# Kernel tuning notes

Measured on AMD Instinct MI355X. Metric: run time of the kernel, lower is better.

The kernel has to match this reference:

```python
import jax, jax.numpy as jnp
import numpy as np


def _three_nn(parent_xyz, xyz):
    # parent_xyz: (bs, n, 3) queries; xyz: (bs, m, 3) reference points.
    # Squared pairwise distances (bs, n, m) without forming (x-y)^2 tensor of rank 4.
    d2 = (jnp.sum(parent_xyz**2, -1, keepdims=True)
          - 2.0 * jnp.einsum('bnd,bmd->bnm', parent_xyz, xyz)
          + jnp.sum(xyz**2, -1)[:, None, :])
    neg_d2, idx = jax.lax.top_k(-d2, 3)           # 3 smallest distances
    dist = jnp.sqrt(jnp.maximum(-neg_d2, 0.0))    # pointnet2 returns sqrt(dist2)
    return dist, idx                              # (bs, n, 3), (bs, n, 3)


def _three_interpolate(feats, idx, weight):
    # feats: (bs, c, m); idx, weight: (bs, n, 3) -> (bs, c, n)
    feats_t = jnp.swapaxes(feats, 1, 2)                     # (bs, m, c)
    gathered = jax.vmap(lambda f, i: f[i])(feats_t, idx)    # (bs, n, 3, c)
    out = jnp.einsum('bnkc,bnk->bcn', gathered, weight)
    return out


def _conv1x1(x, W, b):
    # x: (bs, c_in, n); W: (c_out, c_in); b: (c_out,)
    return jnp.einsum('oc,bcn->bon', W, x) + b[None, :, None]


def setup_inputs() -> dict:
    key = jax.random.key(0)
    ks = jax.random.split(key, 6)
    bs, m, n = 8, 1024, 4096
    c0, c1, c2 = 256, 128, 256
    xyz = jax.random.normal(ks[0], (bs, m, 3), jnp.float32)
    parent_xyz = jax.random.normal(ks[1], (bs, n, 3), jnp.float32)
    feats = jax.random.normal(ks[2], (bs, c0, m), jnp.float32)
    skip_feats = jax.random.normal(ks[3], (bs, c1, n), jnp.float32)
    W1 = jax.random.normal(ks[4], (c2, c0 + c1), jnp.float32) * (1.0 / np.sqrt(c0 + c1))
    b1 = jnp.zeros((c2,), jnp.float32)
    W2 = jax.random.normal(ks[5], (c2, c2), jnp.float32) * (1.0 / np.sqrt(c2))
    b2 = jnp.zeros((c2,), jnp.float32)
    return {"xyz": xyz, "parent_xyz": parent_xyz, "feats": feats,
            "skip_feats": skip_feats, "W1": W1, "b1": b1, "W2": W2, "b2": b2}


def reference(xyz, parent_xyz, feats, skip_feats, W1, b1, W2, b2):
    dist, idx = _three_nn(parent_xyz, xyz)
    inv_dist = 1.0 / (dist + 1e-8)
    weight = inv_dist / jnp.sum(inv_dist, 2, keepdims=True)     # (bs, n, 3)
    up_feats = _three_interpolate(feats, idx, weight)           # (bs, c0, n)
    parent_feats = jnp.concatenate([up_feats, skip_feats], 1)   # (bs, c0+c1, n)
    h = jax.nn.relu(_conv1x1(parent_feats, W1, b1))
    out = jax.nn.relu(_conv1x1(h, W2, b2))
    return out
```

## Files before the change

### kernel.cpp

```cpp
#include <hip/hip_runtime.h>
#include <hip/hip_bf16.h>
#include <cstddef>
#include <cstdint>

#define BS    8
#define M_PTS 1024
#define N_PTS 4096
#define C0    256
#define C1    128
#define C2    256
#define K1DIM 384

typedef __attribute__((ext_vector_type(8))) short bf16x8;
typedef __attribute__((ext_vector_type(4))) float f32x4;

__device__ __forceinline__ ushort f2bf(float f) {
  union { float f; unsigned u; } v; v.f = f;
  unsigned r = v.u + 0x7fffu + ((v.u >> 16) & 1u);
  return (ushort)(r >> 16);
}

__device__ __forceinline__ int pfbu(int kq, int n) {
  return kq * 64 + (n ^ (kq & 7));
}

__global__ void transpose_k(const float* __restrict__ in, float* __restrict__ out,
                            int R, int C) {
  __shared__ float tile[32][33];
  const int b  = blockIdx.z;
  const int r0 = blockIdx.y * 32, c0 = blockIdx.x * 32;
  const int tx = threadIdx.x, ty = threadIdx.y;
  const float* ip = in  + (size_t)b * R * C;
  float*       op = out + (size_t)b * R * C;
#pragma unroll
  for (int i = 0; i < 4; ++i) {
    int r = r0 + ty + i * 8, c = c0 + tx;
    if (r < R && c < C) tile[ty + i * 8][tx] = ip[(size_t)r * C + c];
  }
  __syncthreads();
#pragma unroll
  for (int i = 0; i < 4; ++i) {
    int c = c0 + ty + i * 8, r = r0 + tx;
    if (r < R && c < C) op[(size_t)c * R + r] = tile[tx][ty + i * 8];
  }
}

__global__ __launch_bounds__(256) void wprep_k(
    const float* __restrict__ W1, const float* __restrict__ W2,
    ushort* __restrict__ W1f, ushort* __restrict__ W2f) {
  const int id = blockIdx.x * 256 + threadIdx.x;
  if (id < C2 * K1DIM) {
    int m = id / K1DIM, k = id - m * K1DIM;
    int off = (((m >> 4) * 12 + (k >> 5)) * 4 + ((k >> 3) & 3)) * 128 + (m & 15) * 8 + (k & 7);
    W1f[off] = f2bf(W1[id]);
  }
  if (id < C2 * C2) {
    int m = id >> 8, k = id & 255;
    int off = (((m >> 4) * 8 + (k >> 5)) * 4 + ((k >> 3) & 3)) * 128 + (m & 15) * 8 + (k & 7);
    W2f[off] = f2bf(W2[id]);
  }
}

__global__ __launch_bounds__(512, 4) void fp_fused_k(
    const float* __restrict__ xyz,
    const float* __restrict__ pxyz,
    const float* __restrict__ featsT,
    const float* __restrict__ skip,
    const ushort* __restrict__ W1f,
    const float* __restrict__ b1,
    const ushort* __restrict__ W2f,
    const float* __restrict__ b2,
    float* __restrict__ out) {
  __shared__ float4 smem4[3072];
  __shared__ int   idx_s[64][3];
  __shared__ float w_s[64][3];

  float4* pts = smem4;
  float*  md  = (float*)smem4 + 4128;
  int*    mi  = (int*)smem4  + 4128 + 1536;
  ushort* pfB = (ushort*)smem4;

  const int t  = threadIdx.x;
  const int b  = blockIdx.x & 7;
  const int n0 = (blockIdx.x >> 3) * 64;

  for (int m = t; m < M_PTS; m += 512) {
    const float x = xyz[(size_t)b * 3 * M_PTS + 3 * m + 0];
    const float y = xyz[(size_t)b * 3 * M_PTS + 3 * m + 1];
    const float z = xyz[(size_t)b * 3 * M_PTS + 3 * m + 2];
    const float s2 = __fadd_rn(__fadd_rn(__fmul_rn(x, x), __fmul_rn(y, y)),
                               __fmul_rn(z, z));
    pts[m + (m >> 7)] = (float4){x, y, z, s2};
  }
  __syncthreads();

  float skp[16];
#pragma unroll
  for (int it = 0; it < 8; ++it) {
    const int id = t + it * 512;
    const int r2 = id >> 6, nn = id & 63;
    skp[2 * it + 0] = skip[((size_t)b * C1 + 2 * r2 + 0) * N_PTS + n0 + nn];
    skp[2 * it + 1] = skip[((size_t)b * C1 + 2 * r2 + 1) * N_PTS + n0 + nn];
  }

  {
    const int q = t >> 3, sub = t & 7;
    const int gn = n0 + q;
    const float qx = pxyz[((size_t)b * N_PTS + gn) * 3 + 0];
    const float qy = pxyz[((size_t)b * N_PTS + gn) * 3 + 1];
    const float qz = pxyz[((size_t)b * N_PTS + gn) * 3 + 2];
    const float qq = __fadd_rn(__fadd_rn(__fmul_rn(qx, qx), __fmul_rn(qy, qy)),
                               __fmul_rn(qz, qz));
    float d0 = 3.4e38f, d1 = 3.4e38f, d2 = 3.4e38f;
    int   i0 = 0, i1 = 0, i2 = 0;
    const int mbase = sub * 128;
    const int pbase = mbase + sub;
    for (int it = 0; it < 128; ++it) {
      const float4 P = pts[pbase + it];
      const float dot = __fadd_rn(__fadd_rn(__fmul_rn(qx, P.x), __fmul_rn(qy, P.y)),
                                  __fmul_rn(qz, P.z));
      const float d = __fadd_rn(__fsub_rn(qq, __fmul_rn(2.0f, dot)), P.w);
      const int m = mbase + it;
      if (d < d0)      { d2 = d1; i2 = i1; d1 = d0; i1 = i0; d0 = d; i0 = m; }
      else if (d < d1) { d2 = d1; i2 = i1; d1 = d;  i1 = m; }
      else if (d < d2) { d2 = d;  i2 = m; }
    }
    const int base = (q * 8 + sub) * 3;
    md[base + 0] = d0; md[base + 1] = d1; md[base + 2] = d2;
    mi[base + 0] = i0; mi[base + 1] = i1; mi[base + 2] = i2;

    if (sub == 0) {
      float e0 = 3.4e38f, e1 = 3.4e38f, e2 = 3.4e38f;
      int   j0 = 0, j1 = 0, j2 = 0;
#pragma unroll
      for (int s = 0; s < 8; ++s)
#pragma unroll
        for (int k = 0; k < 3; ++k) {
          float d = md[(q * 8 + s) * 3 + k]; int m = mi[(q * 8 + s) * 3 + k];
          if (d < e0)      { e2 = e1; j2 = j1; e1 = e0; j1 = j0; e0 = d; j0 = m; }
          else if (d < e1) { e2 = e1; j2 = j1; e1 = d;  j1 = m; }
          else if (d < e2) { e2 = d;  j2 = m; }
        }
      float t0 = sqrtf(fmaxf(e0, 0.f)), t1 = sqrtf(fmaxf(e1, 0.f)),
            t2 = sqrtf(fmaxf(e2, 0.f));
      float r0 = 1.0f / (t0 + 1e-8f), r1 = 1.0f / (t1 + 1e-8f),
            r2 = 1.0f / (t2 + 1e-8f);
      float rs = __fadd_rn(__fadd_rn(r0, r1), r2);
      idx_s[q][0] = j0; idx_s[q][1] = j1; idx_s[q][2] = j2;
      w_s[q][0] = r0 / rs; w_s[q][1] = r1 / rs; w_s[q][2] = r2 / rs;
    }
  }
  __syncthreads();

  const int wv = t >> 6, l = t & 63;

  {
    const float* fb = featsT + (size_t)b * M_PTS * C0;
#pragma unroll
    for (int qi = 0; qi < 8; ++qi) {
      const int nq = wv * 8 + qi;
      const float w0 = w_s[nq][0], w1 = w_s[nq][1], w2 = w_s[nq][2];
      const float4 f0 = *(const float4*)(fb + (size_t)idx_s[nq][0] * C0 + l * 4);
      const float4 f1 = *(const float4*)(fb + (size_t)idx_s[nq][1] * C0 + l * 4);
      const float4 f2 = *(const float4*)(fb + (size_t)idx_s[nq][2] * C0 + l * 4);
      ushort4 hv;
      hv.x = f2bf(w0 * f0.x + w1 * f1.x + w2 * f2.x);
      hv.y = f2bf(w0 * f0.y + w1 * f1.y + w2 * f2.y);
      hv.z = f2bf(w0 * f0.z + w1 * f1.z + w2 * f2.z);
      hv.w = f2bf(w0 * f0.w + w1 * f1.w + w2 * f2.w);
      *reinterpret_cast<ushort4*>(&pfB[pfbu(l >> 1, nq) * 8 + (l & 1) * 4]) = hv;
    }
  }
#pragma unroll
  for (int it = 0; it < 8; ++it) {
    const int id = t + it * 512;
    const int r2 = id >> 6, nn = id & 63;
    ushort2 sv; sv.x = f2bf(skp[2 * it]); sv.y = f2bf(skp[2 * it + 1]);
    const int k = C0 + 2 * r2;
    *reinterpret_cast<ushort2*>(&pfB[pfbu(k >> 3, nn) * 8 + (k & 7)]) = sv;
  }
  __syncthreads();

  const int c = l & 15, g = l >> 4;

  f32x4 acc[2][4];
#pragma unroll
  for (int i = 0; i < 2; ++i)
#pragma unroll
    for (int j = 0; j < 4; ++j) acc[i][j] = (f32x4){0.f, 0.f, 0.f, 0.f};

  for (int kb = 0; kb < 12; ++kb) {
    bf16x8 bfr[4], afr[2];
#pragma unroll
    for (int j = 0; j < 4; ++j)
      bfr[j] = *reinterpret_cast<const bf16x8*>(&pfB[pfbu(kb * 4 + g, j * 16 + c) * 8]);
#pragma unroll
    for (int i = 0; i < 2; ++i)
      afr[i] = *reinterpret_cast<const bf16x8*>(&W1f[(((2 * wv + i) * 12 + kb) * 4 + g) * 128 + c * 8]);
#pragma unroll
    for (int i = 0; i < 2; ++i)
#pragma unroll
      for (int j = 0; j < 4; ++j)
        acc[i][j] = __builtin_amdgcn_mfma_f32_16x16x32_bf16(afr[i], bfr[j], acc[i][j], 0, 0, 0);
  }
  __syncthreads();

#pragma unroll
  for (int i = 0; i < 2; ++i) {
    const int mbase = wv * 32 + i * 16 + g * 4;
    const float4 bias = *(const float4*)(b1 + mbase);
#pragma unroll
    for (int j = 0; j < 4; ++j) {
      const int nn = j * 16 + c;
      ushort4 hv;
      hv.x = f2bf(fmaxf(acc[i][j].x + bias.x, 0.f));
      hv.y = f2bf(fmaxf(acc[i][j].y + bias.y, 0.f));
      hv.z = f2bf(fmaxf(acc[i][j].z + bias.z, 0.f));
      hv.w = f2bf(fmaxf(acc[i][j].w + bias.w, 0.f));
      *reinterpret_cast<ushort4*>(&pfB[pfbu(mbase >> 3, nn) * 8 + (mbase & 7)]) = hv;
    }
  }
  __syncthreads();

#pragma unroll
  for (int i = 0; i < 2; ++i)
#pragma unroll
    for (int j = 0; j < 4; ++j) acc[i][j] = (f32x4){0.f, 0.f, 0.f, 0.f};

  for (int kb = 0; kb < 8; ++kb) {
    bf16x8 bfr[4], afr[2];
#pragma unroll
    for (int j = 0; j < 4; ++j)
      bfr[j] = *reinterpret_cast<const bf16x8*>(&pfB[pfbu(kb * 4 + g, j * 16 + c) * 8]);
#pragma unroll
    for (int i = 0; i < 2; ++i)
      afr[i] = *reinterpret_cast<const bf16x8*>(&W2f[(((2 * wv + i) * 8 + kb) * 4 + g) * 128 + c * 8]);
#pragma unroll
    for (int i = 0; i < 2; ++i)
#pragma unroll
      for (int j = 0; j < 4; ++j)
        acc[i][j] = __builtin_amdgcn_mfma_f32_16x16x32_bf16(afr[i], bfr[j], acc[i][j], 0, 0, 0);
  }

#pragma unroll
  for (int i = 0; i < 2; ++i) {
    const int mbase = wv * 32 + i * 16 + g * 4;
    const float4 bias = *(const float4*)(b2 + mbase);
#pragma unroll
    for (int j = 0; j < 4; ++j) {
      const int nn = n0 + j * 16 + c;
      out[((size_t)b * C2 + mbase + 0) * N_PTS + nn] = fmaxf(acc[i][j].x + bias.x, 0.f);
      out[((size_t)b * C2 + mbase + 1) * N_PTS + nn] = fmaxf(acc[i][j].y + bias.y, 0.f);
      out[((size_t)b * C2 + mbase + 2) * N_PTS + nn] = fmaxf(acc[i][j].z + bias.z, 0.f);
      out[((size_t)b * C2 + mbase + 3) * N_PTS + nn] = fmaxf(acc[i][j].w + bias.w, 0.f);
    }
  }
}

extern "C" void kernel_launch(void* const* d_in, const int* in_sizes, int n_in,
                              void* d_out, int out_size, void* d_ws, size_t ws_size,
                              hipStream_t stream) {
  const float* xyz   = (const float*)d_in[0];
  const float* pxyz  = (const float*)d_in[1];
  const float* feats = (const float*)d_in[2];
  const float* skip  = (const float*)d_in[3];
  const float* W1    = (const float*)d_in[4];
  const float* b1    = (const float*)d_in[5];
  const float* W2    = (const float*)d_in[6];
  const float* b2    = (const float*)d_in[7];
  float* out = (float*)d_out;

  float*  ws     = (float*)d_ws;
  float*  featsT = ws;
  ushort* W1f    = (ushort*)(featsT + (size_t)BS * M_PTS * C0);
  ushort* W2f    = W1f + (size_t)C2 * K1DIM;

  dim3 tb(32, 8);
  transpose_k<<<dim3(M_PTS / 32, C0 / 32, BS), tb, 0, stream>>>(feats, featsT, C0, M_PTS);
  wprep_k<<<(C2 * K1DIM) / 256, 256, 0, stream>>>(W1, W2, W1f, W2f);
  fp_fused_k<<<BS * (N_PTS / 64), 512, 0, stream>>>(xyz, pxyz, featsT, skip,
                                                    W1f, b1, W2f, b2, out);
}
```

Baseline: 56.59 us.

## Halve fused tile to 32 points, shuffle-merge top-3, merge prep kernels

The fused kernel now handles 32 query points per 256-thread block instead of 64 per 512, which doubles the grid and reshapes the MFMA tiling to 4x2 per wave. The per-query top-3 merge moves from shared memory with a single-lane serial pass to a butterfly merge over xor shuffles, and neighbour indices and weights are broadcast with readlane instead of going through shared arrays. The point table uses an XOR swizzle with unrolled access in place of padding. The transpose and weight-prep kernels are merged into one launch to cut launch overhead. The trade-offs are more blocks that each reload the 1024 reference points, and higher register pressure from the select-heavy merge.

Measured after the change: 50.10 us. -11.5%, faster.

```diff
diff --git a/kernel.cpp b/kernel.cpp
--- a/kernel.cpp
+++ b/kernel.cpp
@@ -20,48 +20,49 @@
   return (ushort)(r >> 16);
 }
 
-__device__ __forceinline__ int pfbu(int kq, int n) {
-  return kq * 64 + (n ^ (kq & 7));
-}
-
-__global__ void transpose_k(const float* __restrict__ in, float* __restrict__ out,
-                            int R, int C) {
+__device__ __forceinline__ float rdlane_f(float v, int lane) {
+  union { float f; int i; } u; u.f = v;
+  u.i = __builtin_amdgcn_readlane(u.i, lane);
+  return u.f;
+}
+
+__global__ __launch_bounds__(256) void prep_k(
+    const float* __restrict__ feats, const float* __restrict__ W1,
+    const float* __restrict__ W2, float* __restrict__ featsT,
+    ushort* __restrict__ W1f, ushort* __restrict__ W2f) {
   __shared__ float tile[32][33];
-  const int b  = blockIdx.z;
-  const int r0 = blockIdx.y * 32, c0 = blockIdx.x * 32;
-  const int tx = threadIdx.x, ty = threadIdx.y;
-  const float* ip = in  + (size_t)b * R * C;
-  float*       op = out + (size_t)b * R * C;
-#pragma unroll
-  for (int i = 0; i < 4; ++i) {
-    int r = r0 + ty + i * 8, c = c0 + tx;
-    if (r < R && c < C) tile[ty + i * 8][tx] = ip[(size_t)r * C + c];
-  }
-  __syncthreads();
-#pragma unroll
-  for (int i = 0; i < 4; ++i) {
-    int c = c0 + ty + i * 8, r = r0 + tx;
-    if (r < R && c < C) op[(size_t)c * R + r] = tile[tx][ty + i * 8];
-  }
-}
-
-__global__ __launch_bounds__(256) void wprep_k(
-    const float* __restrict__ W1, const float* __restrict__ W2,
-    ushort* __restrict__ W1f, ushort* __restrict__ W2f) {
-  const int id = blockIdx.x * 256 + threadIdx.x;
-  if (id < C2 * K1DIM) {
-    int m = id / K1DIM, k = id - m * K1DIM;
-    int off = (((m >> 4) * 12 + (k >> 5)) * 4 + ((k >> 3) & 3)) * 128 + (m & 15) * 8 + (k & 7);
-    W1f[off] = f2bf(W1[id]);
-  }
-  if (id < C2 * C2) {
-    int m = id >> 8, k = id & 255;
-    int off = (((m >> 4) * 8 + (k >> 5)) * 4 + ((k >> 3) & 3)) * 128 + (m & 15) * 8 + (k & 7);
-    W2f[off] = f2bf(W2[id]);
-  }
-}
-
-__global__ __launch_bounds__(512, 4) void fp_fused_k(
+  const int t = threadIdx.x;
+  if (blockIdx.x < 2048) {
+    const int bx = blockIdx.x & 31;
+    const int by = (blockIdx.x >> 5) & 7;
+    const int bz = blockIdx.x >> 8;
+    const int tx = t & 31, ty = t >> 5;
+    const float* ip = feats + (size_t)bz * C0 * M_PTS;
+    float*       op = featsT + (size_t)bz * C0 * M_PTS;
+    const int r0 = by * 32, c0 = bx * 32;
+#pragma unroll
+    for (int i = 0; i < 4; ++i)
+      tile[ty + i * 8][tx] = ip[(size_t)(r0 + ty + i * 8) * M_PTS + c0 + tx];
+    __syncthreads();
+#pragma unroll
+    for (int i = 0; i < 4; ++i)
+      op[(size_t)(c0 + ty + i * 8) * C0 + r0 + tx] = tile[tx][ty + i * 8];
+  } else {
+    const int id = (blockIdx.x - 2048) * 256 + t;
+    if (id < C2 * K1DIM) {
+      int m = id / K1DIM, k = id - m * K1DIM;
+      int off = (((m >> 4) * 12 + (k >> 5)) * 4 + ((k >> 3) & 3)) * 128 + (m & 15) * 8 + (k & 7);
+      W1f[off] = f2bf(W1[id]);
+    }
+    if (id < C2 * C2) {
+      int m = id >> 8, k = id & 255;
+      int off = (((m >> 4) * 8 + (k >> 5)) * 4 + ((k >> 3) & 3)) * 128 + (m & 15) * 8 + (k & 7);
+      W2f[off] = f2bf(W2[id]);
+    }
+  }
+}
+
+__global__ __launch_bounds__(256, 4) void fp_fused_k(
     const float* __restrict__ xyz,
     const float* __restrict__ pxyz,
     const float* __restrict__ featsT,
@@ -71,183 +72,203 @@
     const ushort* __restrict__ W2f,
     const float* __restrict__ b2,
     float* __restrict__ out) {
-  __shared__ float4 smem4[3072];
-  __shared__ int   idx_s[64][3];
-  __shared__ float w_s[64][3];
-
-  float4* pts = smem4;
-  float*  md  = (float*)smem4 + 4128;
-  int*    mi  = (int*)smem4  + 4128 + 1536;
-  ushort* pfB = (ushort*)smem4;
+  __shared__ float4 smemq[2560];
+  float4* pts4 = smemq;
+  ushort* pfB  = (ushort*)(smemq + 1024);
+  ushort* hbuf = (ushort*)smemq;
 
   const int t  = threadIdx.x;
   const int b  = blockIdx.x & 7;
-  const int n0 = (blockIdx.x >> 3) * 64;
-
-  for (int m = t; m < M_PTS; m += 512) {
+  const int n0 = (blockIdx.x >> 3) * 32;
+  const int wv = t >> 6, l = t & 63;
+  const int q  = t >> 3, sub = t & 7;
+
+  const float qx = pxyz[((size_t)b * N_PTS + n0 + q) * 3 + 0];
+  const float qy = pxyz[((size_t)b * N_PTS + n0 + q) * 3 + 1];
+  const float qz = pxyz[((size_t)b * N_PTS + n0 + q) * 3 + 2];
+
+#pragma unroll
+  for (int it = 0; it < 4; ++it) {
+    const int m = t + it * 256;
     const float x = xyz[(size_t)b * 3 * M_PTS + 3 * m + 0];
     const float y = xyz[(size_t)b * 3 * M_PTS + 3 * m + 1];
     const float z = xyz[(size_t)b * 3 * M_PTS + 3 * m + 2];
     const float s2 = __fadd_rn(__fadd_rn(__fmul_rn(x, x), __fmul_rn(y, y)),
                                __fmul_rn(z, z));
-    pts[m + (m >> 7)] = (float4){x, y, z, s2};
-  }
-  __syncthreads();
+    pts4[m ^ ((m >> 7) & 7)] = (float4){x, y, z, s2};
+  }
 
   float skp[16];
 #pragma unroll
   for (int it = 0; it < 8; ++it) {
-    const int id = t + it * 512;
-    const int r2 = id >> 6, nn = id & 63;
+    const int id = t + it * 256;
+    const int r2 = id >> 5, nn = id & 31;
     skp[2 * it + 0] = skip[((size_t)b * C1 + 2 * r2 + 0) * N_PTS + n0 + nn];
     skp[2 * it + 1] = skip[((size_t)b * C1 + 2 * r2 + 1) * N_PTS + n0 + nn];
   }
 
+  const float qq = __fadd_rn(__fadd_rn(__fmul_rn(qx, qx), __fmul_rn(qy, qy)),
+                             __fmul_rn(qz, qz));
+  __syncthreads();
+
+  float d0 = 3.4e38f, d1 = 3.4e38f, d2 = 3.4e38f;
+  int   i0 = 0, i1 = 0, i2 = 0;
   {
-    const int q = t >> 3, sub = t & 7;
-    const int gn = n0 + q;
-    const float qx = pxyz[((size_t)b * N_PTS + gn) * 3 + 0];
-    const float qy = pxyz[((size_t)b * N_PTS + gn) * 3 + 1];
-    const float qz = pxyz[((size_t)b * N_PTS + gn) * 3 + 2];
-    const float qq = __fadd_rn(__fadd_rn(__fmul_rn(qx, qx), __fmul_rn(qy, qy)),
-                               __fmul_rn(qz, qz));
-    float d0 = 3.4e38f, d1 = 3.4e38f, d2 = 3.4e38f;
-    int   i0 = 0, i1 = 0, i2 = 0;
-    const int mbase = sub * 128;
-    const int pbase = mbase + sub;
-    for (int it = 0; it < 128; ++it) {
-      const float4 P = pts[pbase + it];
-      const float dot = __fadd_rn(__fadd_rn(__fmul_rn(qx, P.x), __fmul_rn(qy, P.y)),
-                                  __fmul_rn(qz, P.z));
-      const float d = __fadd_rn(__fsub_rn(qq, __fmul_rn(2.0f, dot)), P.w);
-      const int m = mbase + it;
-      if (d < d0)      { d2 = d1; i2 = i1; d1 = d0; i1 = i0; d0 = d; i0 = m; }
-      else if (d < d1) { d2 = d1; i2 = i1; d1 = d;  i1 = m; }
-      else if (d < d2) { d2 = d;  i2 = m; }
-    }
-    const int base = (q * 8 + sub) * 3;
-    md[base + 0] = d0; md[base + 1] = d1; md[base + 2] = d2;
-    mi[base + 0] = i0; mi[base + 1] = i1; mi[base + 2] = i2;
-
-    if (sub == 0) {
-      float e0 = 3.4e38f, e1 = 3.4e38f, e2 = 3.4e38f;
-      int   j0 = 0, j1 = 0, j2 = 0;
-#pragma unroll
-      for (int s = 0; s < 8; ++s)
-#pragma unroll
-        for (int k = 0; k < 3; ++k) {
-          float d = md[(q * 8 + s) * 3 + k]; int m = mi[(q * 8 + s) * 3 + k];
-          if (d < e0)      { e2 = e1; j2 = j1; e1 = e0; j1 = j0; e0 = d; j0 = m; }
-          else if (d < e1) { e2 = e1; j2 = j1; e1 = d;  j1 = m; }
-          else if (d < e2) { e2 = d;  j2 = m; }
-        }
-      float t0 = sqrtf(fmaxf(e0, 0.f)), t1 = sqrtf(fmaxf(e1, 0.f)),
-            t2 = sqrtf(fmaxf(e2, 0.f));
-      float r0 = 1.0f / (t0 + 1e-8f), r1 = 1.0f / (t1 + 1e-8f),
-            r2 = 1.0f / (t2 + 1e-8f);
-      float rs = __fadd_rn(__fadd_rn(r0, r1), r2);
-      idx_s[q][0] = j0; idx_s[q][1] = j1; idx_s[q][2] = j2;
-      w_s[q][0] = r0 / rs; w_s[q][1] = r1 / rs; w_s[q][2] = r2 / rs;
-    }
-  }
-  __syncthreads();
-
-  const int wv = t >> 6, l = t & 63;
+    const float4* pblk = pts4 + sub * 128;
+    for (int a = 0; a < 16; ++a) {
+#pragma unroll
+      for (int e = 0; e < 8; ++e) {
+        const float4 P = pblk[(a << 3) + (e ^ sub)];
+        const float dot = __fadd_rn(__fadd_rn(__fmul_rn(qx, P.x), __fmul_rn(qy, P.y)),
+                                    __fmul_rn(qz, P.z));
+        const float d = __fadd_rn(__fsub_rn(qq, __fmul_rn(2.0f, dot)), P.w);
+        const int m = sub * 128 + (a << 3) + e;
+        if (d < d0)      { d2 = d1; i2 = i1; d1 = d0; i1 = i0; d0 = d; i0 = m; }
+        else if (d < d1) { d2 = d1; i2 = i1; d1 = d;  i1 = m; }
+        else if (d < d2) { d2 = d;  i2 = m; }
+      }
+    }
+  }
+
+#pragma unroll
+  for (int mk = 1; mk <= 4; mk <<= 1) {
+    const float pd0 = __shfl_xor(d0, mk), pd1 = __shfl_xor(d1, mk), pd2 = __shfl_xor(d2, mk);
+    const int   pi0 = __shfl_xor(i0, mk), pi1 = __shfl_xor(i1, mk), pi2 = __shfl_xor(i2, mk);
+    const bool lo = (sub & mk) == 0;
+    const float a0 = lo ? d0 : pd0, a1 = lo ? d1 : pd1, a2 = lo ? d2 : pd2;
+    const float b0 = lo ? pd0 : d0, b1v = lo ? pd1 : d1, b2v = lo ? pd2 : d2;
+    const int   A0 = lo ? i0 : pi0, A1 = lo ? i1 : pi1, A2 = lo ? i2 : pi2;
+    const int   B0 = lo ? pi0 : i0, B1 = lo ? pi1 : i1, B2 = lo ? pi2 : i2;
+    const bool c0 = b0 < a0;
+    const bool cb1a0 = b1v < a0, cb0a1 = b0 < a1;
+    const bool cb1a1 = b1v < a1, cb2a0 = b2v < a0, cb0a2 = b0 < a2;
+    const float m0 = c0 ? b0 : a0;                 const int M0 = c0 ? B0 : A0;
+    const float t1a = cb1a0 ? b1v : a0;            const int T1a = cb1a0 ? B1 : A0;
+    const float t1b = cb0a1 ? b0 : a1;             const int T1b = cb0a1 ? B0 : A1;
+    const float m1 = c0 ? t1a : t1b;               const int M1 = c0 ? T1a : T1b;
+    const float sA = cb2a0 ? b2v : a0;             const int SA = cb2a0 ? B2 : A0;
+    const float sB = cb1a1 ? b1v : a1;             const int SB = cb1a1 ? B1 : A1;
+    const float sD = cb0a2 ? b0 : a2;              const int SD = cb0a2 ? B0 : A2;
+    const float m2 = c0 ? (cb1a0 ? sA : sB) : (cb0a1 ? sB : sD);
+    const int   M2 = c0 ? (cb1a0 ? SA : SB) : (cb0a1 ? SB : SD);
+    d0 = m0; d1 = m1; d2 = m2; i0 = M0; i1 = M1; i2 = M2;
+  }
+
+  float w0f, w1f, w2f;
+  {
+    const float t0 = sqrtf(fmaxf(d0, 0.f)), t1 = sqrtf(fmaxf(d1, 0.f)),
+                t2 = sqrtf(fmaxf(d2, 0.f));
+    const float r0 = 1.0f / (t0 + 1e-8f), r1 = 1.0f / (t1 + 1e-8f),
+                r2 = 1.0f / (t2 + 1e-8f);
+    const float rs = __fadd_rn(__fadd_rn(r0, r1), r2);
+    w0f = r0 / rs; w1f = r1 / rs; w2f = r2 / rs;
+  }
 
   {
     const float* fb = featsT + (size_t)b * M_PTS * C0;
 #pragma unroll
     for (int qi = 0; qi < 8; ++qi) {
-      const int nq = wv * 8 + qi;
-      const float w0 = w_s[nq][0], w1 = w_s[nq][1], w2 = w_s[nq][2];
-      const float4 f0 = *(const float4*)(fb + (size_t)idx_s[nq][0] * C0 + l * 4);
-      const float4 f1 = *(const float4*)(fb + (size_t)idx_s[nq][1] * C0 + l * 4);
-      const float4 f2 = *(const float4*)(fb + (size_t)idx_s[nq][2] * C0 + l * 4);
+      const int src = qi * 8;
+      const int  j0 = __builtin_amdgcn_readlane(i0, src);
+      const int  j1 = __builtin_amdgcn_readlane(i1, src);
+      const int  j2 = __builtin_amdgcn_readlane(i2, src);
+      const float w0 = rdlane_f(w0f, src), w1 = rdlane_f(w1f, src), w2 = rdlane_f(w2f, src);
+      const float4 f0 = *(const float4*)(fb + (size_t)j0 * C0 + l * 4);
+      const float4 f1 = *(const float4*)(fb + (size_t)j1 * C0 + l * 4);
+      const float4 f2 = *(const float4*)(fb + (size_t)j2 * C0 + l * 4);
       ushort4 hv;
       hv.x = f2bf(w0 * f0.x + w1 * f1.x + w2 * f2.x);
       hv.y = f2bf(w0 * f0.y + w1 * f1.y + w2 * f2.y);
       hv.z = f2bf(w0 * f0.z + w1 * f1.z + w2 * f2.z);
       hv.w = f2bf(w0 * f0.w + w1 * f1.w + w2 * f2.w);
-      *reinterpret_cast<ushort4*>(&pfB[pfbu(l >> 1, nq) * 8 + (l & 1) * 4]) = hv;
+      const int nq = wv * 8 + qi;
+      const int kq = l >> 1;
+      const int u = kq * 32 + (nq ^ (kq & 7));
+      *reinterpret_cast<ushort4*>(&pfB[u * 8 + (l & 1) * 4]) = hv;
     }
   }
 #pragma unroll
   for (int it = 0; it < 8; ++it) {
-    const int id = t + it * 512;
-    const int r2 = id >> 6, nn = id & 63;
+    const int id = t + it * 256;
+    const int r2 = id >> 5, nn = id & 31;
+    const int k = C0 + 2 * r2;
+    const int kq = k >> 3;
+    const int u = kq * 32 + (nn ^ (kq & 7));
     ushort2 sv; sv.x = f2bf(skp[2 * it]); sv.y = f2bf(skp[2 * it + 1]);
-    const int k = C0 + 2 * r2;
-    *reinterpret_cast<ushort2*>(&pfB[pfbu(k >> 3, nn) * 8 + (k & 7)]) = sv;
+    *reinterpret_cast<ushort2*>(&pfB[u * 8 + (k & 7)]) = sv;
   }
   __syncthreads();
 
   const int c = l & 15, g = l >> 4;
 
-  f32x4 acc[2][4];
-#pragma unroll
-  for (int i = 0; i < 2; ++i)
-#pragma unroll
-    for (int j = 0; j < 4; ++j) acc[i][j] = (f32x4){0.f, 0.f, 0.f, 0.f};
+  f32x4 acc[4][2];
+#pragma unroll
+  for (int i = 0; i < 4; ++i)
+#pragma unroll
+    for (int j = 0; j < 2; ++j) acc[i][j] = (f32x4){0.f, 0.f, 0.f, 0.f};
 
   for (int kb = 0; kb < 12; ++kb) {
-    bf16x8 bfr[4], afr[2];
-#pragma unroll
-    for (int j = 0; j < 4; ++j)
-      bfr[j] = *reinterpret_cast<const bf16x8*>(&pfB[pfbu(kb * 4 + g, j * 16 + c) * 8]);
-#pragma unroll
-    for (int i = 0; i < 2; ++i)
-      afr[i] = *reinterpret_cast<const bf16x8*>(&W1f[(((2 * wv + i) * 12 + kb) * 4 + g) * 128 + c * 8]);
-#pragma unroll
-    for (int i = 0; i < 2; ++i)
-#pragma unroll
-      for (int j = 0; j < 4; ++j)
+    const int kqg = kb * 4 + g;
+    bf16x8 bfr[2], afr[4];
+#pragma unroll
+    for (int j = 0; j < 2; ++j)
+      bfr[j] = *reinterpret_cast<const bf16x8*>(&pfB[(kqg * 32 + ((j * 16 + c) ^ (kqg & 7))) * 8]);
+#pragma unroll
+    for (int i = 0; i < 4; ++i)
+      afr[i] = *reinterpret_cast<const bf16x8*>(&W1f[(((wv * 4 + i) * 12 + kb) * 4 + g) * 128 + c * 8]);
+#pragma unroll
+    for (int i = 0; i < 4; ++i)
+#pragma unroll
+      for (int j = 0; j < 2; ++j)
         acc[i][j] = __builtin_amdgcn_mfma_f32_16x16x32_bf16(afr[i], bfr[j], acc[i][j], 0, 0, 0);
   }
-  __syncthreads();
-
-#pragma unroll
-  for (int i = 0; i < 2; ++i) {
-    const int mbase = wv * 32 + i * 16 + g * 4;
+
+#pragma unroll
+  for (int i = 0; i < 4; ++i) {
+    const int mbase = wv * 64 + i * 16 + g * 4;
     const float4 bias = *(const float4*)(b1 + mbase);
 #pragma unroll
-    for (int j = 0; j < 4; ++j) {
+    for (int j = 0; j < 2; ++j) {
       const int nn = j * 16 + c;
+      const int kq = mbase >> 3;
+      const int u = kq * 32 + (nn ^ (kq & 7));
       ushort4 hv;
       hv.x = f2bf(fmaxf(acc[i][j].x + bias.x, 0.f));
       hv.y = f2bf(fmaxf(acc[i][j].y + bias.y, 0.f));
       hv.z = f2bf(fmaxf(acc[i][j].z + bias.z, 0.f));
       hv.w = f2bf(fmaxf(acc[i][j].w + bias.w, 0.f));
-      *reinterpret_cast<ushort4*>(&pfB[pfbu(mbase >> 3, nn) * 8 + (mbase & 7)]) = hv;
+      *reinterpret_cast<ushort4*>(&hbuf[u * 8 + (mbase & 7)]) = hv;
     }
   }
   __syncthreads();
 
 #pragma unroll
-  for (int i = 0; i < 2; ++i)
-#pragma unroll
-    for (int j = 0; j < 4; ++j) acc[i][j] = (f32x4){0.f, 0.f, 0.f, 0.f};
+  for (int i = 0; i < 4; ++i)
+#pragma unroll
+    for (int j = 0; j < 2; ++j) acc[i][j] = (f32x4){0.f, 0.f, 0.f, 0.f};
 
   for (int kb = 0; kb < 8; ++kb) {
-    bf16x8 bfr[4], afr[2];
-#pragma unroll
-    for (int j = 0; j < 4; ++j)
-      bfr[j] = *reinterpret_cast<const bf16x8*>(&pfB[pfbu(kb * 4 + g, j * 16 + c) * 8]);
-#pragma unroll
-    for (int i = 0; i < 2; ++i)
-      afr[i] = *reinterpret_cast<const bf16x8*>(&W2f[(((2 * wv + i) * 8 + kb) * 4 + g) * 128 + c * 8]);
-#pragma unroll
-    for (int i = 0; i < 2; ++i)
-#pragma unroll
-      for (int j = 0; j < 4; ++j)
+    const int kqg = kb * 4 + g;
+    bf16x8 bfr[2], afr[4];
+#pragma unroll
+    for (int j = 0; j < 2; ++j)
+      bfr[j] = *reinterpret_cast<const bf16x8*>(&hbuf[(kqg * 32 + ((j * 16 + c) ^ (kqg & 7))) * 8]);
+#pragma unroll
+    for (int i = 0; i < 4; ++i)
+      afr[i] = *reinterpret_cast<const bf16x8*>(&W2f[(((wv * 4 + i) * 8 + kb) * 4 + g) * 128 + c * 8]);
+#pragma unroll
+    for (int i = 0; i < 4; ++i)
+#pragma unroll
+      for (int j = 0; j < 2; ++j)
         acc[i][j] = __builtin_amdgcn_mfma_f32_16x16x32_bf16(afr[i], bfr[j], acc[i][j], 0, 0, 0);
   }
 
 #pragma unroll
-  for (int i = 0; i < 2; ++i) {
-    const int mbase = wv * 32 + i * 16 + g * 4;
+  for (int i = 0; i < 4; ++i) {
+    const int mbase = wv * 64 + i * 16 + g * 4;
     const float4 bias = *(const float4*)(b2 + mbase);
 #pragma unroll
-    for (int j = 0; j < 4; ++j) {
+    for (int j = 0; j < 2; ++j) {
       const int nn = n0 + j * 16 + c;
       out[((size_t)b * C2 + mbase + 0) * N_PTS + nn] = fmaxf(acc[i][j].x + bias.x, 0.f);
       out[((size_t)b * C2 + mbase + 1) * N_PTS + nn] = fmaxf(acc[i][j].y + bias.y, 0.f);
@@ -275,9 +296,7 @@
   ushort* W1f    = (ushort*)(featsT + (size_t)BS * M_PTS * C0);
   ushort* W2f    = W1f + (size_t)C2 * K1DIM;
 
-  dim3 tb(32, 8);
-  transpose_k<<<dim3(M_PTS / 32, C0 / 32, BS), tb, 0, stream>>>(feats, featsT, C0, M_PTS);
-  wprep_k<<<(C2 * K1DIM) / 256, 256, 0, stream>>>(W1, W2, W1f, W2f);
-  fp_fused_k<<<BS * (N_PTS / 64), 512, 0, stream>>>(xyz, pxyz, featsT, skip,
+  prep_k<<<2432, 256, 0, stream>>>(feats, W1, W2, featsT, W1f, W2f);
+  fp_fused_k<<<BS * (N_PTS / 32), 256, 0, stream>>>(xyz, pxyz, featsT, skip,
                                                     W1f, b1, W2f, b2, out);
 }
```
